# Kernel optimization log

Measured on AMD Instinct MI355X. Metric: run time of the kernel, lower is better.

## Reference

```python
import jax, jax.numpy as jnp
import numpy as np


def setup_inputs() -> dict:
    key = jax.random.key(0)
    kx, ks = jax.random.split(key)
    x = jax.random.normal(kx, (64, 128, 56, 56), dtype=jnp.float32)
    # scale must be nonnegative (asserted in torch forward); uniform (0,1)
    scale = jax.random.uniform(ks, (15,), dtype=jnp.float32, minval=0.05, maxval=1.0)
    return {
        "x": x,
        "scale": scale,
        "Qn": 0,
        "Qp": 15,
        "num_elements": 64 * 128 * 56 * 56,
        "box_size": 1024 * 256,
    }


def reference(x, scale, Qn, Qp, num_elements, box_size):
    # cumulative level boundaries (non-uniform quantization grid)
    cumsum_scale = jnp.cumsum(scale)                      # [Qp]
    # bucketize: midpoint boundaries (cumsum - scale/2), side='left' matches
    # torch.searchsorted(right=False)
    idx1 = jnp.searchsorted(cumsum_scale - scale * 0.5, x)  # [*x.shape]
    levels = jnp.concatenate([jnp.zeros((1,), x.dtype), cumsum_scale])  # [Qp+1]
    y = levels[idx1]
    return y
```

## Files before the change

### kernel.cpp

```cpp
#include <hip/hip_runtime.h>
#include <hip/hip_bf16.h>


typedef float vfloat4 __attribute__((ext_vector_type(4)));

__device__ __forceinline__ unsigned qidx_asm(float x, const float* __restrict__ b) {
    unsigned idx;
    asm("v_mov_b32 %0, 0\n\t"
        "v_cmp_lt_f32 vcc, %1, %16\n\t"
        "v_addc_co_u32 %0, vcc, %0, 0, vcc\n\t"
        "v_cmp_lt_f32 vcc, %2, %16\n\t"
        "v_addc_co_u32 %0, vcc, %0, 0, vcc\n\t"
        "v_cmp_lt_f32 vcc, %3, %16\n\t"
        "v_addc_co_u32 %0, vcc, %0, 0, vcc\n\t"
        "v_cmp_lt_f32 vcc, %4, %16\n\t"
        "v_addc_co_u32 %0, vcc, %0, 0, vcc\n\t"
        "v_cmp_lt_f32 vcc, %5, %16\n\t"
        "v_addc_co_u32 %0, vcc, %0, 0, vcc\n\t"
        "v_cmp_lt_f32 vcc, %6, %16\n\t"
        "v_addc_co_u32 %0, vcc, %0, 0, vcc\n\t"
        "v_cmp_lt_f32 vcc, %7, %16\n\t"
        "v_addc_co_u32 %0, vcc, %0, 0, vcc\n\t"
        "v_cmp_lt_f32 vcc, %8, %16\n\t"
        "v_addc_co_u32 %0, vcc, %0, 0, vcc\n\t"
        "v_cmp_lt_f32 vcc, %9, %16\n\t"
        "v_addc_co_u32 %0, vcc, %0, 0, vcc\n\t"
        "v_cmp_lt_f32 vcc, %10, %16\n\t"
        "v_addc_co_u32 %0, vcc, %0, 0, vcc\n\t"
        "v_cmp_lt_f32 vcc, %11, %16\n\t"
        "v_addc_co_u32 %0, vcc, %0, 0, vcc\n\t"
        "v_cmp_lt_f32 vcc, %12, %16\n\t"
        "v_addc_co_u32 %0, vcc, %0, 0, vcc\n\t"
        "v_cmp_lt_f32 vcc, %13, %16\n\t"
        "v_addc_co_u32 %0, vcc, %0, 0, vcc\n\t"
        "v_cmp_lt_f32 vcc, %14, %16\n\t"
        "v_addc_co_u32 %0, vcc, %0, 0, vcc\n\t"
        "v_cmp_lt_f32 vcc, %15, %16\n\t"
        "v_addc_co_u32 %0, vcc, %0, 0, vcc"
        : "=&v"(idx)
        : "v"(b[0]), "v"(b[1]), "v"(b[2]), "v"(b[3]), "v"(b[4]),
          "v"(b[5]), "v"(b[6]), "v"(b[7]), "v"(b[8]), "v"(b[9]),
          "v"(b[10]), "v"(b[11]), "v"(b[12]), "v"(b[13]), "v"(b[14]),
          "v"(x)
        : "vcc");
    return idx;
}

__global__ __launch_bounds__(256) void nulsq_quant_kernel(
    const float* __restrict__ x, const float* __restrict__ scale,
    float* __restrict__ y, int n4, int n, int full_blocks) {
#pragma clang fp contract(off)
    __shared__ float levels[16];

    float b[15];
    {
        float c = 0.0f;
#pragma unroll
        for (int j = 0; j < 15; ++j) {
            float s = scale[j];
            c = c + s;
            b[j] = c - s * 0.5f;
        }
    }
    if (threadIdx.x == 0) {
        float c = 0.0f;
        levels[0] = 0.0f;
#pragma unroll
        for (int j = 0; j < 15; ++j) {
            c = c + scale[j];
            levels[j + 1] = c;
        }
    }
    __syncthreads();

    const vfloat4* __restrict__ x4 = reinterpret_cast<const vfloat4*>(x);
    vfloat4* __restrict__ y4 = reinterpret_cast<vfloat4*>(y);

    const int bx = (int)blockIdx.x;
    const int base = bx * 1024 + (int)threadIdx.x;

    if (bx < full_blocks) {
        vfloat4 v0 = x4[base];
        vfloat4 v1 = x4[base + 256];
        vfloat4 v2 = x4[base + 512];
        vfloat4 v3 = x4[base + 768];

        vfloat4 r;
        r.x = levels[qidx_asm(v0.x, b)];
        r.y = levels[qidx_asm(v0.y, b)];
        r.z = levels[qidx_asm(v0.z, b)];
        r.w = levels[qidx_asm(v0.w, b)];
        y4[base] = r;

        r.x = levels[qidx_asm(v1.x, b)];
        r.y = levels[qidx_asm(v1.y, b)];
        r.z = levels[qidx_asm(v1.z, b)];
        r.w = levels[qidx_asm(v1.w, b)];
        y4[base + 256] = r;

        r.x = levels[qidx_asm(v2.x, b)];
        r.y = levels[qidx_asm(v2.y, b)];
        r.z = levels[qidx_asm(v2.z, b)];
        r.w = levels[qidx_asm(v2.w, b)];
        y4[base + 512] = r;

        r.x = levels[qidx_asm(v3.x, b)];
        r.y = levels[qidx_asm(v3.y, b)];
        r.z = levels[qidx_asm(v3.z, b)];
        r.w = levels[qidx_asm(v3.w, b)];
        y4[base + 768] = r;
    } else {
#pragma unroll
        for (int k = 0; k < 4; ++k) {
            int fi = base + k * 256;
            if (fi < n4) {
                vfloat4 v = x4[fi];
                vfloat4 r;
                r.x = levels[qidx_asm(v.x, b)];
                r.y = levels[qidx_asm(v.y, b)];
                r.z = levels[qidx_asm(v.z, b)];
                r.w = levels[qidx_asm(v.w, b)];
                y4[fi] = r;
            }
        }
        int tail = n - n4 * 4;
        if ((int)threadIdx.x < tail && bx == full_blocks) {
            int i = n4 * 4 + (int)threadIdx.x;
            y[i] = levels[qidx_asm(x[i], b)];
        }
    }
}

extern "C" void kernel_launch(void* const* d_in, const int* in_sizes, int n_in,
                              void* d_out, int out_size, void* d_ws, size_t ws_size,
                              hipStream_t stream) {
    const float* x = (const float*)d_in[0];
    const float* scale = (const float*)d_in[1];
    float* y = (float*)d_out;

    int n = in_sizes[0];
    int n4 = n / 4;

    const int block = 256;
    const int f4_per_block = block * 4;
    int full_blocks = n4 / f4_per_block;
    int grid = (n4 + f4_per_block - 1) / f4_per_block;
    if (n - n4 * 4 > 0 && grid == full_blocks) grid += 1;
    if (grid < 1) grid = 1;

    nulsq_quant_kernel<<<grid, block, 0, stream>>>(x, scale, y, n4, n, full_blocks);
}
```

Measured before the change: 189.4 us.

## Issue eight inline-asm dwordx4 loads per thread with staged vmcnt waits

Doubles the work per block to 8 float4s per thread and remaps indices so each wave owns a contiguous 512-float4 region. All eight loads are issued up front as inline-asm global_load_dwordx4 with immediate offsets, and each chunk waits on an incremental vmcnt, so compute on early chunks overlaps the later loads. Stores also use inline asm. This adds register pressure, halves the block count, and hand-written waitcnt that the compiler cannot reason about. The tail handling moves to the last block.

```diff
diff --git a/kernel.cpp b/kernel.cpp
--- a/kernel.cpp
+++ b/kernel.cpp
@@ -46,6 +46,18 @@
     return idx;
 }
 
+#define LOADK(dst, base, OFF)                                               \
+    asm volatile("global_load_dwordx4 %0, %1, off offset:" #OFF             \
+                 : "=v"(dst) : "v"(base))
+
+#define WAITV(N, reg)                                                       \
+    asm volatile("s_waitcnt vmcnt(" #N ")" : "+v"(reg)::"memory");          \
+    __builtin_amdgcn_sched_barrier(0)
+
+#define STOREK(src, base, OFF)                                              \
+    asm volatile("global_store_dwordx4 %0, %1, off offset:" #OFF            \
+                 :: "v"(base), "v"(src) : "memory")
+
 __global__ __launch_bounds__(256) void nulsq_quant_kernel(
     const float* __restrict__ x, const float* __restrict__ scale,
     float* __restrict__ y, int n4, int n, int full_blocks) {
@@ -77,57 +89,60 @@
     vfloat4* __restrict__ y4 = reinterpret_cast<vfloat4*>(y);
 
     const int bx = (int)blockIdx.x;
-    const int base = bx * 1024 + (int)threadIdx.x;
+    const int wave = (int)threadIdx.x >> 6;
+    const int lane = (int)threadIdx.x & 63;
+    const int f4base = bx * 2048 + wave * 512 + lane;
 
     if (bx < full_blocks) {
-        vfloat4 v0 = x4[base];
-        vfloat4 v1 = x4[base + 256];
-        vfloat4 v2 = x4[base + 512];
-        vfloat4 v3 = x4[base + 768];
+        const vfloat4* px0 = x4 + f4base;
+        const vfloat4* px4 = px0 + 256;
+        vfloat4* py0 = y4 + f4base;
+        vfloat4* py4 = py0 + 256;
+
+        vfloat4 v0, v1, v2, v3, v4, v5, v6, v7;
+        LOADK(v0, px0, 0);
+        LOADK(v1, px0, 1024);
+        LOADK(v2, px0, 2048);
+        LOADK(v3, px0, 3072);
+        LOADK(v4, px4, 0);
+        LOADK(v5, px4, 1024);
+        LOADK(v6, px4, 2048);
+        LOADK(v7, px4, 3072);
 
         vfloat4 r;
-        r.x = levels[qidx_asm(v0.x, b)];
-        r.y = levels[qidx_asm(v0.y, b)];
-        r.z = levels[qidx_asm(v0.z, b)];
-        r.w = levels[qidx_asm(v0.w, b)];
-        y4[base] = r;
+#define CHUNK(vk, pb, OFF)                        \
+        r.x = levels[qidx_asm(vk.x, b)];          \
+        r.y = levels[qidx_asm(vk.y, b)];          \
+        r.z = levels[qidx_asm(vk.z, b)];          \
+        r.w = levels[qidx_asm(vk.w, b)];          \
+        STOREK(r, pb, OFF)
 
-        r.x = levels[qidx_asm(v1.x, b)];
-        r.y = levels[qidx_asm(v1.y, b)];
-        r.z = levels[qidx_asm(v1.z, b)];
-        r.w = levels[qidx_asm(v1.w, b)];
-        y4[base + 256] = r;
+        WAITV(7, v0); CHUNK(v0, py0, 0);
+        WAITV(6, v1); CHUNK(v1, py0, 1024);
+        WAITV(5, v2); CHUNK(v2, py0, 2048);
+        WAITV(4, v3); CHUNK(v3, py0, 3072);
+        WAITV(3, v4); CHUNK(v4, py4, 0);
+        WAITV(2, v5); CHUNK(v5, py4, 1024);
+        WAITV(1, v6); CHUNK(v6, py4, 2048);
+        WAITV(0, v7); CHUNK(v7, py4, 3072);
+#undef CHUNK
+    } else {
+        int end = (bx + 1) * 2048;
+        if (end > n4) end = n4;
+        for (int i = bx * 2048 + (int)threadIdx.x; i < end; i += 256) {
+            vfloat4 v = x4[i];
+            vfloat4 r;
+            r.x = levels[qidx_asm(v.x, b)];
+            r.y = levels[qidx_asm(v.y, b)];
+            r.z = levels[qidx_asm(v.z, b)];
+            r.w = levels[qidx_asm(v.w, b)];
+            y4[i] = r;
+        }
+    }
 
-        r.x = levels[qidx_asm(v2.x, b)];
-        r.y = levels[qidx_asm(v2.y, b)];
-        r.z = levels[qidx_asm(v2.z, b)];
-        r.w = levels[qidx_asm(v2.w, b)];
-        y4[base + 512] = r;
-
-        r.x = levels[qidx_asm(v3.x, b)];
-        r.y = levels[qidx_asm(v3.y, b)];
-        r.z = levels[qidx_asm(v3.z, b)];
-        r.w = levels[qidx_asm(v3.w, b)];
-        y4[base + 768] = r;
-    } else {
-#pragma unroll
-        for (int k = 0; k < 4; ++k) {
-            int fi = base + k * 256;
-            if (fi < n4) {
-                vfloat4 v = x4[fi];
-                vfloat4 r;
-                r.x = levels[qidx_asm(v.x, b)];
-                r.y = levels[qidx_asm(v.y, b)];
-                r.z = levels[qidx_asm(v.z, b)];
-                r.w = levels[qidx_asm(v.w, b)];
-                y4[fi] = r;
-            }
-        }
-        int tail = n - n4 * 4;
-        if ((int)threadIdx.x < tail && bx == full_blocks) {
-            int i = n4 * 4 + (int)threadIdx.x;
-            y[i] = levels[qidx_asm(x[i], b)];
-        }
+    if (bx == (int)gridDim.x - 1) {
+        int t = n4 * 4 + (int)threadIdx.x;
+        if (t < n) y[t] = levels[qidx_asm(x[t], b)];
     }
 }
 
@@ -142,10 +157,9 @@
     int n4 = n / 4;
 
     const int block = 256;
-    const int f4_per_block = block * 4;
+    const int f4_per_block = block * 8;
     int full_blocks = n4 / f4_per_block;
     int grid = (n4 + f4_per_block - 1) / f4_per_block;
-    if (n - n4 * 4 > 0 && grid == full_blocks) grid += 1;
     if (grid < 1) grid = 1;
 
     nulsq_quant_kernel<<<grid, block, 0, stream>>>(x, scale, y, n4, n, full_blocks);
```

Measured after the change: 192.1 us. No clear change (+1.4%).
